# Performance work log

Hardware: AMD Instinct MI355X
Metric: run time of the kernel (lower is better)

The kernel has to match this reference:

```python
import jax, jax.numpy as jnp
import numpy as np

INF = 1.0e6  # 'infinity' for squared EDT; max real value is ~3*128^2 ~ 5e4


def edt_1d_sq(f, axis):
    """One pass of Felzenszwalb separable squared EDT along `axis`.
    d[i] = min_j f[j] + (i - j)^2  (brute-force vectorized lower envelope)."""
    f = jnp.moveaxis(f, axis, -1)
    n = f.shape[-1]
    i = jnp.arange(n, dtype=f.dtype)
    sq = (i[:, None] - i[None, :]) ** 2  # (n, n)
    d = jnp.min(f[..., None, :] + sq, axis=-1)  # (..., n)
    return jnp.moveaxis(d, -1, axis)


def compute_fg_dtm(mask):
    """Euclidean distance transform of foreground (distance to nearest background),
    matching scipy.ndimage.distance_transform_edt applied per batch element on the
    (C, X, Y, Z) mask (C==1 so the channel axis pass is the identity).
    mask: bool (B, 1, X, Y, Z) -> float32 (B, 1, X, Y, Z)."""
    def per_b(m):
        g = jnp.where(m, jnp.float32(INF), jnp.float32(0.0))
        for ax in range(m.ndim):
            g = edt_1d_sq(g, ax)
        return jnp.sqrt(g)
    return jax.lax.map(per_b, mask)


def setup_inputs() -> dict:
    key = jax.random.key(0)
    k1, k2, k3 = jax.random.split(key, 3)
    B, C, X, Y, Z = 2, 2, 128, 128, 128
    return {
        "outputs": jax.random.normal(k1, (B, C, X, Y, Z), dtype=jnp.float32),
        "outputs_dist": jax.random.normal(k2, (B, C, X, Y, Z), dtype=jnp.float32) * 10.0,
        "y": jax.random.randint(k3, (B, 1, X, Y, Z), 0, 2),
        "distance_map_weight": 1.0,
    }


def reference(outputs, outputs_dist, y, distance_map_weight):
    n_pred_ch = outputs.shape[1]
    # MONAI one_hot: (B,1,X,Y,Z) int labels -> (B,C,X,Y,Z) float
    y1h = jnp.moveaxis(jax.nn.one_hot(y[:, 0], n_pred_ch, dtype=outputs.dtype), -1, 1)
    x = outputs[:, 1:]            # foreground logits (B, 1, X, Y, Z)
    t = y1h[:, 1:]                # foreground mask
    od = outputs_dist[:, 1:]
    gt_dis = compute_fg_dtm(t > 0.5)
    # BCE with logits (mean reduction), numerically stable
    loss_ce = jnp.mean(jnp.maximum(x, 0.0) - x * t + jnp.log1p(jnp.exp(-jnp.abs(x))))
    # dice loss, flattened per batch element
    N = x.shape[0]
    smooth = jnp.float32(1.0)
    p = jax.nn.sigmoid(x).reshape(N, -1)
    tf = t.reshape(N, -1)
    dice = (2.0 * jnp.sum(p * tf, axis=1) + smooth) / (jnp.sum(p, axis=1) + jnp.sum(tf, axis=1) + smooth)
    loss_dice = 1.0 - jnp.sum(dice) / N
    # weighted L1 on the distance head, masked by the foreground mask
    msum = jnp.sum(t)
    loss_dist = jnp.where(
        msum == 0,
        jnp.float32(0.0),
        jnp.sum(jnp.abs(od - gt_dis) * t) / jnp.maximum(msum, jnp.float32(1e-12)),
    )
    return loss_ce + loss_dice + distance_map_weight * loss_dist
```

## Files before the change

### kernel.cpp

```cpp
#include <hip/hip_runtime.h>
#include <math.h>

#define M_SPATIAL 2097152

__device__ __forceinline__ float wave_redf(float v) {
#pragma unroll
  for (int o = 32; o > 0; o >>= 1) v += __shfl_down(v, o, 64);
  return v;
}
__device__ __forceinline__ double wave_redd(double v) {
#pragma unroll
  for (int o = 32; o > 0; o >>= 1) v += __shfl_down(v, o, 64);
  return v;
}
__device__ __forceinline__ float min3f(float a, float b, float c) {
  float d;
  asm("v_min3_f32 %0, %1, %2, %3" : "=v"(d) : "v"(a), "v"(b), "v"(c));
  return d;
}


__global__ __launch_bounds__(256) void kAB(const int* __restrict__ y,
                                           const float* __restrict__ outputs,
                                           float* __restrict__ g,
                                           double* __restrict__ part) {
  int blk = blockIdx.x;
  int b  = blk >> 9;
  int yy = (blk >> 2) & 127;
  int zq = blk & 3;
  int t  = threadIdx.x;
  int c  = t >> 5;
  int zl = t & 31;
  int x0 = c * 16;
  size_t sp   = (size_t)yy * 128 + (size_t)zq * 32 + zl;
  size_t base = (size_t)b * M_SPATIAL + sp;
  const float* xc = outputs + (size_t)(b * 2 + 1) * M_SPATIAL;

  int yb[16];
  float xv[16];
#pragma unroll
  for (int k = 0; k < 16; ++k) yb[k] = y[base + (size_t)(x0 + k) * 16384];
#pragma unroll
  for (int k = 0; k < 16; ++k) xv[k] = xc[sp + (size_t)(x0 + k) * 16384];

  int lastE = -200, nextE = 400;
#pragma unroll
  for (int k = 0; k < 16; ++k) lastE = (yb[k] == 1) ? lastE : (x0 + k);
#pragma unroll
  for (int k = 15; k >= 0; --k) nextE = (yb[k] == 1) ? nextE : (x0 + k);

  __shared__ int lE[8][32];
  __shared__ int nE[8][32];
  lE[c][zl] = lastE;
  nE[c][zl] = nextE;
  __syncthreads();

  int carryL = -200, carryN = 400;
#pragma unroll
  for (int q = 0; q < 7; ++q) {
    if (q < c)     carryL = max(carryL, lE[q][zl]);
    if (q + 1 > c) carryN = min(carryN, nE[q + 1][zl]);
  }

  float yy2f = (float)(yy * yy);
  float hinf = 1000000.f + yy2f;

  int df[16];
  int ll = carryL;
#pragma unroll
  for (int k = 0; k < 16; ++k) {
    ll = (yb[k] == 1) ? ll : (x0 + k);
    df[k] = min(x0 + k - ll, 200);
  }
  float ov[16];
  int nn = carryN;
#pragma unroll
  for (int k = 15; k >= 0; --k) {
    nn = (yb[k] == 1) ? nn : (x0 + k);
    int m = min(df[k], min(nn - (x0 + k), 200));
    ov[k] = (m >= 128) ? hinf : ((float)(m * m) + yy2f);
  }
#pragma unroll
  for (int k = 0; k < 16; ++k) g[base + (size_t)(x0 + k) * 16384] = ov[k];

  float ce = 0.f, ps = 0.f, pts = 0.f, tsum = 0.f;
#pragma unroll
  for (int k = 0; k < 16; ++k) {
    float tt = (yb[k] == 1) ? 1.0f : 0.0f;
    float xx = xv[k];
    ce += fmaxf(xx, 0.0f) - xx * tt + log1pf(expf(-fabsf(xx)));
    float p = 1.0f / (1.0f + expf(-xx));
    ps += p; pts += p * tt; tsum += tt;
  }
  float r0 = wave_redf(ce), r1 = wave_redf(ps), r2 = wave_redf(pts), r3 = wave_redf(tsum);
  __shared__ float sm[4][4];
  int lane = t & 63, w = t >> 6;
  if (lane == 0) { sm[w][0] = r0; sm[w][1] = r1; sm[w][2] = r2; sm[w][3] = r3; }
  __syncthreads();
  if (t == 0) {
    part[blk]        = (double)(sm[0][0] + sm[1][0] + sm[2][0] + sm[3][0]);
    part[1024 + blk] = (double)(sm[0][1] + sm[1][1] + sm[2][1] + sm[3][1]);
    part[2048 + blk] = (double)(sm[0][2] + sm[1][2] + sm[2][2] + sm[3][2]);
    part[3072 + blk] = (double)(sm[0][3] + sm[1][3] + sm[2][3] + sm[3][3]);
  }
}

__global__ __launch_bounds__(512, 1) void kCD(const float* __restrict__ g,
                                              const float* __restrict__ od,
                                              double* __restrict__ part) {
  __shared__ float hl[144 * 129];
  __shared__ float sred[8];
  int blk = blockIdx.x;
  int b = blk >> 7, xx = blk & 127;
  int t = threadIdx.x;
  size_t rb = (size_t)b * M_SPATIAL + (size_t)xx * 16384;

  for (int idx = t; idx < 8 * 129; idx += 512) {
    hl[idx] = 1.0e9f;
    hl[136 * 129 + idx] = 1.0e9f;
  }
  const float4* g4 = (const float4*)(g + rb);
#pragma unroll
  for (int r = 0; r < 8; ++r) {
    int i4 = t + r * 512;
    float4 v = g4[i4];
    int yy = i4 >> 5, z4 = (i4 & 31) * 4;
    float* p = &hl[(yy + 8) * 129 + z4];
    p[0] = v.x; p[1] = v.y; p[2] = v.z; p[3] = v.w;
  }
  __syncthreads();

  int zcol = t & 127, ig = t >> 7;
  float dvy[2][16];
#pragma unroll
  for (int cb = 0; cb < 2; ++cb) {
    int ibase = ig * 32 + cb * 16;
    float best[16], mc[16];
#pragma unroll
    for (int k = 0; k < 16; ++k) {
      best[k] = 3.0e38f;
      mc[k] = -2.0f * (float)(ibase + k);
    }
    float jb = (float)(ibase - 8);
#pragma unroll 4
    for (int p = 0; p < 16; ++p) {
      float h0 = hl[(ibase + 2 * p) * 129 + zcol];
      float h1 = hl[(ibase + 2 * p + 1) * 129 + zcol];
      float j0 = jb + (float)(2 * p), j1 = jb + (float)(2 * p + 1);
#pragma unroll
      for (int k = 0; k < 16; ++k) {
        float v0 = fmaf(mc[k], j0, h0);
        float v1 = fmaf(mc[k], j1, h1);
        best[k] = min3f(v0, v1, best[k]);
      }
    }
    int ok = 1;
#pragma unroll
    for (int k = 0; k < 16; ++k) {
      int i = ibase + k;
      dvy[cb][k] = (float)(i * i) + best[k];
      float bnd = (float)min((k + 9) * (k + 9), (24 - k) * (24 - k));
      ok &= (dvy[cb][k] <= bnd);
    }
    if (!__all(ok)) {
#pragma unroll
      for (int k = 0; k < 16; ++k) best[k] = 3.0e38f;
#pragma unroll 2
      for (int j = 0; j < 128; j += 2) {
        float h0 = hl[(j + 8) * 129 + zcol];
        float h1 = hl[(j + 9) * 129 + zcol];
        float j0 = (float)j, j1 = (float)(j + 1);
#pragma unroll
        for (int k = 0; k < 16; ++k) {
          float v0 = fmaf(mc[k], j0, h0);
          float v1 = fmaf(mc[k], j1, h1);
          best[k] = min3f(v0, v1, best[k]);
        }
      }
#pragma unroll
      for (int k = 0; k < 16; ++k) {
        int i = ibase + k;
        dvy[cb][k] = (float)(i * i) + best[k];
      }
    }
  }
  __syncthreads();
  {
    float zq = (float)(zcol * zcol);
#pragma unroll
    for (int cb = 0; cb < 2; ++cb) {
      int ibase = ig * 32 + cb * 16;
#pragma unroll
      for (int k = 0; k < 16; ++k)
        hl[(zcol + 8) * 129 + (ibase + k)] = dvy[cb][k] + zq;
    }
  }
  __syncthreads();

  int ycol = t & 127, izg = t >> 7;
  size_t odb = (size_t)(2 * b + 1) * M_SPATIAL + (size_t)xx * 16384 +
               (size_t)ycol * 128 + (size_t)izg * 32;
  const float4* o4 = (const float4*)(od + odb);
  float4 ovv[8];
#pragma unroll
  for (int r = 0; r < 8; ++r) ovv[r] = o4[r];
  const float* of = (const float*)ovv;

  float dist = 0.f;
#pragma unroll
  for (int cb = 0; cb < 2; ++cb) {
    int izb = izg * 32 + cb * 16;
    float best[16], mc[16];
#pragma unroll
    for (int k = 0; k < 16; ++k) {
      best[k] = 3.0e38f;
      mc[k] = -2.0f * (float)(izb + k);
    }
    float jb = (float)(izb - 8);
#pragma unroll 4
    for (int p = 0; p < 16; ++p) {
      float h0 = hl[(izb + 2 * p) * 129 + ycol];
      float h1 = hl[(izb + 2 * p + 1) * 129 + ycol];
      float j0 = jb + (float)(2 * p), j1 = jb + (float)(2 * p + 1);
#pragma unroll
      for (int k = 0; k < 16; ++k) {
        float v0 = fmaf(mc[k], j0, h0);
        float v1 = fmaf(mc[k], j1, h1);
        best[k] = min3f(v0, v1, best[k]);
      }
    }
    float dv[16];
    int ok = 1;
#pragma unroll
    for (int k = 0; k < 16; ++k) {
      int i = izb + k;
      dv[k] = (float)(i * i) + best[k];
      float bnd = (float)min((k + 9) * (k + 9), (24 - k) * (24 - k));
      ok &= (dv[k] <= bnd);
    }
    if (!__all(ok)) {
#pragma unroll
      for (int k = 0; k < 16; ++k) best[k] = 3.0e38f;
#pragma unroll 2
      for (int j = 0; j < 128; j += 2) {
        float h0 = hl[(j + 8) * 129 + ycol];
        float h1 = hl[(j + 9) * 129 + ycol];
        float j0 = (float)j, j1 = (float)(j + 1);
#pragma unroll
        for (int k = 0; k < 16; ++k) {
          float v0 = fmaf(mc[k], j0, h0);
          float v1 = fmaf(mc[k], j1, h1);
          best[k] = min3f(v0, v1, best[k]);
        }
      }
#pragma unroll
      for (int k = 0; k < 16; ++k) {
        int i = izb + k;
        dv[k] = (float)(i * i) + best[k];
      }
    }
#pragma unroll
    for (int k = 0; k < 16; ++k) {
      if (dv[k] > 0.f) dist += fabsf(of[cb * 16 + k] - sqrtf(dv[k]));
    }
  }
  float r = wave_redf(dist);
  int lane = t & 63, w = t >> 6;
  if (lane == 0) sred[w] = r;
  __syncthreads();
  if (t == 0) {
    float s = 0.f;
#pragma unroll
    for (int q = 0; q < 8; ++q) s += sred[q];
    part[4096 + blk] = (double)s;
  }
}

__global__ __launch_bounds__(256) void k_final(const double* __restrict__ part,
                                               const float* __restrict__ wptr,
                                               float* __restrict__ out) {
  int i = threadIdx.x;
  double ce  = part[i] + part[i + 256] + part[i + 512] + part[i + 768];
  double p0  = part[1024 + i] + part[1024 + i + 256];
  double p1  = part[1536 + i] + part[1536 + i + 256];
  double pt0 = part[2048 + i] + part[2048 + i + 256];
  double pt1 = part[2560 + i] + part[2560 + i + 256];
  double t0  = part[3072 + i] + part[3072 + i + 256];
  double t1  = part[3584 + i] + part[3584 + i + 256];
  double ds  = part[4096 + i];

  ce = wave_redd(ce); p0 = wave_redd(p0); p1 = wave_redd(p1);
  pt0 = wave_redd(pt0); pt1 = wave_redd(pt1);
  t0 = wave_redd(t0); t1 = wave_redd(t1); ds = wave_redd(ds);

  __shared__ double sm[4][8];
  int lane = threadIdx.x & 63, w = threadIdx.x >> 6;
  if (lane == 0) {
    sm[w][0] = ce; sm[w][1] = p0; sm[w][2] = p1; sm[w][3] = pt0;
    sm[w][4] = pt1; sm[w][5] = t0; sm[w][6] = t1; sm[w][7] = ds;
  }
  __syncthreads();
  if (threadIdx.x == 0) {
    double a[8];
    for (int q = 0; q < 8; ++q) a[q] = sm[0][q] + sm[1][q] + sm[2][q] + sm[3][q];
    double cem = a[0] / 4194304.0;
    double dice0 = (2.0 * a[3] + 1.0) / (a[1] + a[5] + 1.0);
    double dice1 = (2.0 * a[4] + 1.0) / (a[2] + a[6] + 1.0);
    double ldice = 1.0 - 0.5 * (dice0 + dice1);
    double msum = a[5] + a[6];
    double ldist = (msum == 0.0) ? 0.0 : a[7] / fmax(msum, 1e-12);
    out[0] = (float)(cem + ldice + (double)wptr[0] * ldist);
  }
}

extern "C" void kernel_launch(void* const* d_in, const int* in_sizes, int n_in,
                              void* d_out, int out_size, void* d_ws, size_t ws_size,
                              hipStream_t stream) {
  const float* outputs      = (const float*)d_in[0];
  const float* outputs_dist = (const float*)d_in[1];
  const int*   y            = (const int*)d_in[2];
  const float* wptr         = (const float*)d_in[3];
  float* out = (float*)d_out;

  double* part = (double*)d_ws;
  float* g = (float*)((char*)d_ws + 65536);

  kAB<<<1024, 256, 0, stream>>>(y, outputs, g, part);
  kCD<<<256, 512, 0, stream>>>(g, outputs_dist, part);
  k_final<<<1, 256, 0, stream>>>(part, wptr, out);
}
```

Measured before the change: 139.1 us.

## Stage x-pass tiles through LDS with vectorized loads and transposed intermediate layout

kAB now loads y and logits as int4/float4 contiguous along z, stages labels in shared memory, runs the x-axis scan from LDS, and writes the intermediate as float4 in a (b, y, x, z) transposed layout. kCD reads from that transposed layout. The grid is halved with each block covering 64 z columns. The goal is to replace strided scalar global accesses with coalesced vector accesses. The cost is a large shared buffer, which may reduce occupancy, plus extra barriers.

Measured after the change: 200.6 us. +44.2%, slower.

```diff
diff --git a/kernel.cpp b/kernel.cpp
--- a/kernel.cpp
+++ b/kernel.cpp
@@ -2,6 +2,7 @@
 #include <math.h>
 
 #define M_SPATIAL 2097152
+#define MV4 (M_SPATIAL / 4)
 
 __device__ __forceinline__ float wave_redf(float v) {
 #pragma unroll
@@ -20,44 +21,64 @@
 }
 
 
-__global__ __launch_bounds__(256) void kAB(const int* __restrict__ y,
-                                           const float* __restrict__ outputs,
-                                           float* __restrict__ g,
-                                           double* __restrict__ part) {
+__global__ __launch_bounds__(256, 2) void kAB(const int* __restrict__ y,
+                                              const float* __restrict__ outputs,
+                                              float* __restrict__ gT,
+                                              double* __restrict__ part) {
+  __shared__ int ysl[128 * 68];
+  __shared__ int lE[4][64];
+  __shared__ int nE[4][64];
+  __shared__ float sm[4][4];
   int blk = blockIdx.x;
-  int b  = blk >> 9;
-  int yy = (blk >> 2) & 127;
-  int zq = blk & 3;
+  int b  = blk >> 8;
+  int yy = (blk >> 1) & 127;
+  int zh = blk & 1;
   int t  = threadIdx.x;
-  int c  = t >> 5;
-  int zl = t & 31;
-  int x0 = c * 16;
-  size_t sp   = (size_t)yy * 128 + (size_t)zq * 32 + zl;
-  size_t base = (size_t)b * M_SPATIAL + sp;
-  const float* xc = outputs + (size_t)(b * 2 + 1) * M_SPATIAL;
-
-  int yb[16];
-  float xv[16];
-#pragma unroll
-  for (int k = 0; k < 16; ++k) yb[k] = y[base + (size_t)(x0 + k) * 16384];
-#pragma unroll
-  for (int k = 0; k < 16; ++k) xv[k] = xc[sp + (size_t)(x0 + k) * 16384];
+
+  const int4*   y4  = (const int4*)y;
+  const float4* xc4 = (const float4*)outputs + (size_t)(b * 2 + 1) * MV4;
+
+  float ce = 0.f, ps = 0.f, pts = 0.f, tsum = 0.f;
+#pragma unroll
+  for (int r = 0; r < 8; ++r) {
+    int i4 = t + r * 256;
+    int x  = i4 >> 4;
+    int u  = i4 & 15;
+    size_t sp4 = (size_t)x * 4096 + (size_t)yy * 32 + (size_t)zh * 16 + u;
+    int4  yv = y4[(size_t)b * MV4 + sp4];
+    float4 xv = xc4[sp4];
+#define ELEM(cc, yc)                                                        \
+    {                                                                       \
+      float tt = (yc == 1) ? 1.0f : 0.0f;                                   \
+      float xx = xv.cc;                                                     \
+      ce += fmaxf(xx, 0.0f) - xx * tt + log1pf(expf(-fabsf(xx)));           \
+      float p = 1.0f / (1.0f + expf(-xx));                                  \
+      ps += p; pts += p * tt; tsum += tt;                                   \
+    }
+    ELEM(x, yv.x) ELEM(y, yv.y) ELEM(z, yv.z) ELEM(w, yv.w)
+#undef ELEM
+    *(int4*)&ysl[x * 68 + u * 4] = yv;
+  }
+  __syncthreads();
+
+  int zl = t & 63, c = t >> 6;
+  int x0 = c * 32;
+  int yb[32];
+#pragma unroll
+  for (int k = 0; k < 32; ++k) yb[k] = ysl[(x0 + k) * 68 + zl];
 
   int lastE = -200, nextE = 400;
 #pragma unroll
-  for (int k = 0; k < 16; ++k) lastE = (yb[k] == 1) ? lastE : (x0 + k);
-#pragma unroll
-  for (int k = 15; k >= 0; --k) nextE = (yb[k] == 1) ? nextE : (x0 + k);
-
-  __shared__ int lE[8][32];
-  __shared__ int nE[8][32];
+  for (int k = 0; k < 32; ++k) lastE = (yb[k] == 1) ? lastE : (x0 + k);
+#pragma unroll
+  for (int k = 31; k >= 0; --k) nextE = (yb[k] == 1) ? nextE : (x0 + k);
   lE[c][zl] = lastE;
   nE[c][zl] = nextE;
   __syncthreads();
 
   int carryL = -200, carryN = 400;
 #pragma unroll
-  for (int q = 0; q < 7; ++q) {
+  for (int q = 0; q < 3; ++q) {
     if (q < c)     carryL = max(carryL, lE[q][zl]);
     if (q + 1 > c) carryN = min(carryN, nE[q + 1][zl]);
   }
@@ -65,47 +86,47 @@
   float yy2f = (float)(yy * yy);
   float hinf = 1000000.f + yy2f;
 
-  int df[16];
+  int df[32];
   int ll = carryL;
 #pragma unroll
-  for (int k = 0; k < 16; ++k) {
+  for (int k = 0; k < 32; ++k) {
     ll = (yb[k] == 1) ? ll : (x0 + k);
     df[k] = min(x0 + k - ll, 200);
   }
-  float ov[16];
+  float* hsl = (float*)ysl;
   int nn = carryN;
 #pragma unroll
-  for (int k = 15; k >= 0; --k) {
+  for (int k = 31; k >= 0; --k) {
     nn = (yb[k] == 1) ? nn : (x0 + k);
     int m = min(df[k], min(nn - (x0 + k), 200));
-    ov[k] = (m >= 128) ? hinf : ((float)(m * m) + yy2f);
-  }
-#pragma unroll
-  for (int k = 0; k < 16; ++k) g[base + (size_t)(x0 + k) * 16384] = ov[k];
-
-  float ce = 0.f, ps = 0.f, pts = 0.f, tsum = 0.f;
-#pragma unroll
-  for (int k = 0; k < 16; ++k) {
-    float tt = (yb[k] == 1) ? 1.0f : 0.0f;
-    float xx = xv[k];
-    ce += fmaxf(xx, 0.0f) - xx * tt + log1pf(expf(-fabsf(xx)));
-    float p = 1.0f / (1.0f + expf(-xx));
-    ps += p; pts += p * tt; tsum += tt;
-  }
+    hsl[(x0 + k) * 68 + zl] = (m >= 128) ? hinf : ((float)(m * m) + yy2f);
+  }
+  __syncthreads();
+
+  float4* gT4 = (float4*)gT;
+#pragma unroll
+  for (int r = 0; r < 8; ++r) {
+    int i4 = t + r * 256;
+    int x  = i4 >> 4;
+    int u  = i4 & 15;
+    float4 v = *(float4*)&hsl[x * 68 + u * 4];
+    gT4[(size_t)b * MV4 + (size_t)yy * 4096 + (size_t)x * 32 +
+        (size_t)zh * 16 + u] = v;
+  }
+
   float r0 = wave_redf(ce), r1 = wave_redf(ps), r2 = wave_redf(pts), r3 = wave_redf(tsum);
-  __shared__ float sm[4][4];
   int lane = t & 63, w = t >> 6;
   if (lane == 0) { sm[w][0] = r0; sm[w][1] = r1; sm[w][2] = r2; sm[w][3] = r3; }
   __syncthreads();
   if (t == 0) {
     part[blk]        = (double)(sm[0][0] + sm[1][0] + sm[2][0] + sm[3][0]);
-    part[1024 + blk] = (double)(sm[0][1] + sm[1][1] + sm[2][1] + sm[3][1]);
-    part[2048 + blk] = (double)(sm[0][2] + sm[1][2] + sm[2][2] + sm[3][2]);
-    part[3072 + blk] = (double)(sm[0][3] + sm[1][3] + sm[2][3] + sm[3][3]);
-  }
-}
-
-__global__ __launch_bounds__(512, 1) void kCD(const float* __restrict__ g,
+    part[512 + blk]  = (double)(sm[0][1] + sm[1][1] + sm[2][1] + sm[3][1]);
+    part[1024 + blk] = (double)(sm[0][2] + sm[1][2] + sm[2][2] + sm[3][2]);
+    part[1536 + blk] = (double)(sm[0][3] + sm[1][3] + sm[2][3] + sm[3][3]);
+  }
+}
+
+__global__ __launch_bounds__(512, 1) void kCD(const float* __restrict__ gT,
                                               const float* __restrict__ od,
                                               double* __restrict__ part) {
   __shared__ float hl[144 * 129];
@@ -113,19 +134,18 @@
   int blk = blockIdx.x;
   int b = blk >> 7, xx = blk & 127;
   int t = threadIdx.x;
-  size_t rb = (size_t)b * M_SPATIAL + (size_t)xx * 16384;
 
   for (int idx = t; idx < 8 * 129; idx += 512) {
     hl[idx] = 1.0e9f;
     hl[136 * 129 + idx] = 1.0e9f;
   }
-  const float4* g4 = (const float4*)(g + rb);
+  const float4* gT4 = (const float4*)gT;
 #pragma unroll
   for (int r = 0; r < 8; ++r) {
     int i4 = t + r * 512;
-    float4 v = g4[i4];
-    int yy = i4 >> 5, z4 = (i4 & 31) * 4;
-    float* p = &hl[(yy + 8) * 129 + z4];
+    int yyi = i4 >> 5, u = i4 & 31;
+    float4 v = gT4[(size_t)b * MV4 + (size_t)yyi * 4096 + (size_t)xx * 32 + u];
+    float* p = &hl[(yyi + 8) * 129 + u * 4];
     p[0] = v.x; p[1] = v.y; p[2] = v.z; p[3] = v.w;
   }
   __syncthreads();
@@ -272,7 +292,7 @@
     float s = 0.f;
 #pragma unroll
     for (int q = 0; q < 8; ++q) s += sred[q];
-    part[4096 + blk] = (double)s;
+    part[2048 + blk] = (double)s;
   }
 }
 
@@ -280,14 +300,14 @@
                                                const float* __restrict__ wptr,
                                                float* __restrict__ out) {
   int i = threadIdx.x;
-  double ce  = part[i] + part[i + 256] + part[i + 512] + part[i + 768];
-  double p0  = part[1024 + i] + part[1024 + i + 256];
-  double p1  = part[1536 + i] + part[1536 + i + 256];
-  double pt0 = part[2048 + i] + part[2048 + i + 256];
-  double pt1 = part[2560 + i] + part[2560 + i + 256];
-  double t0  = part[3072 + i] + part[3072 + i + 256];
-  double t1  = part[3584 + i] + part[3584 + i + 256];
-  double ds  = part[4096 + i];
+  double ce  = part[i] + part[i + 256];
+  double p0  = part[512 + i];
+  double p1  = part[768 + i];
+  double pt0 = part[1024 + i];
+  double pt1 = part[1280 + i];
+  double t0  = part[1536 + i];
+  double t1  = part[1792 + i];
+  double ds  = part[2048 + i];
 
   ce = wave_redd(ce); p0 = wave_redd(p0); p1 = wave_redd(p1);
   pt0 = wave_redd(pt0); pt1 = wave_redd(pt1);
@@ -323,9 +343,9 @@
   float* out = (float*)d_out;
 
   double* part = (double*)d_ws;
-  float* g = (float*)((char*)d_ws + 65536);
-
-  kAB<<<1024, 256, 0, stream>>>(y, outputs, g, part);
-  kCD<<<256, 512, 0, stream>>>(g, outputs_dist, part);
+  float* gT = (float*)((char*)d_ws + 65536);
+
+  kAB<<<512, 256, 0, stream>>>(y, outputs, gT, part);
+  kCD<<<256, 512, 0, stream>>>(gT, outputs_dist, part);
   k_final<<<1, 256, 0, stream>>>(part, wptr, out);
 }
```

## Stage kAB loads through shared memory with vectorized int4/float4 and transposed g layout

Applied to the files above, without the earlier changes.

kAB now loads y and logits as int4/float4 vectors into a shared tile, computes the BCE/dice partial sums on the vector loads, and runs the x-axis EDT from shared memory. It writes the intermediate g in a (y, x, z) transposed layout through shared memory with float4 stores, and kCD reads it with the matching indexing. The intent is to replace scalar loads and stores strided by 16384 along x with wide coalesced accesses. The cost is extra shared memory (about 18 KB per block) and an extra barrier, and kCD's reads now hit 128-byte segments strided by yy instead of contiguous rows.

Result: slower. 206.0 us (+48.1%).

```diff
diff --git a/kernel.cpp b/kernel.cpp
--- a/kernel.cpp
+++ b/kernel.cpp
@@ -2,6 +2,7 @@
 #include <math.h>
 
 #define M_SPATIAL 2097152
+#define MV4 (M_SPATIAL / 4)
 
 __device__ __forceinline__ float wave_redf(float v) {
 #pragma unroll
@@ -20,37 +21,57 @@
 }
 
 
-__global__ __launch_bounds__(256) void kAB(const int* __restrict__ y,
-                                           const float* __restrict__ outputs,
-                                           float* __restrict__ g,
-                                           double* __restrict__ part) {
+__global__ __launch_bounds__(256, 4) void kAB(const int* __restrict__ y,
+                                              const float* __restrict__ outputs,
+                                              float* __restrict__ gT,
+                                              double* __restrict__ part) {
+  __shared__ int ysl[128 * 36];
+  __shared__ int lE[8][32];
+  __shared__ int nE[8][32];
+  __shared__ float sm[4][4];
   int blk = blockIdx.x;
   int b  = blk >> 9;
   int yy = (blk >> 2) & 127;
   int zq = blk & 3;
   int t  = threadIdx.x;
-  int c  = t >> 5;
-  int zl = t & 31;
+
+  const int4*   y4  = (const int4*)y;
+  const float4* xc4 = (const float4*)outputs + (size_t)(b * 2 + 1) * MV4;
+
+  float ce = 0.f, ps = 0.f, pts = 0.f, tsum = 0.f;
+#pragma unroll
+  for (int r = 0; r < 4; ++r) {
+    int i4 = t + r * 256;
+    int x  = i4 >> 3;
+    int u  = i4 & 7;
+    size_t sp4 = (size_t)x * 4096 + (size_t)yy * 32 + (size_t)zq * 8 + u;
+    int4  yv = y4[(size_t)b * MV4 + sp4];
+    float4 xv = xc4[sp4];
+#define ELEM(cc, yc)                                                        \
+    {                                                                       \
+      float tt = (yc == 1) ? 1.0f : 0.0f;                                   \
+      float xx = xv.cc;                                                     \
+      ce += fmaxf(xx, 0.0f) - xx * tt + log1pf(expf(-fabsf(xx)));           \
+      float p = 1.0f / (1.0f + expf(-xx));                                  \
+      ps += p; pts += p * tt; tsum += tt;                                   \
+    }
+    ELEM(x, yv.x) ELEM(y, yv.y) ELEM(z, yv.z) ELEM(w, yv.w)
+#undef ELEM
+    *(int4*)&ysl[x * 36 + u * 4] = yv;
+  }
+  __syncthreads();
+
+  int zl = t & 31, c = t >> 5;
   int x0 = c * 16;
-  size_t sp   = (size_t)yy * 128 + (size_t)zq * 32 + zl;
-  size_t base = (size_t)b * M_SPATIAL + sp;
-  const float* xc = outputs + (size_t)(b * 2 + 1) * M_SPATIAL;
-
   int yb[16];
-  float xv[16];
-#pragma unroll
-  for (int k = 0; k < 16; ++k) yb[k] = y[base + (size_t)(x0 + k) * 16384];
-#pragma unroll
-  for (int k = 0; k < 16; ++k) xv[k] = xc[sp + (size_t)(x0 + k) * 16384];
+#pragma unroll
+  for (int k = 0; k < 16; ++k) yb[k] = ysl[(x0 + k) * 36 + zl];
 
   int lastE = -200, nextE = 400;
 #pragma unroll
   for (int k = 0; k < 16; ++k) lastE = (yb[k] == 1) ? lastE : (x0 + k);
 #pragma unroll
   for (int k = 15; k >= 0; --k) nextE = (yb[k] == 1) ? nextE : (x0 + k);
-
-  __shared__ int lE[8][32];
-  __shared__ int nE[8][32];
   lE[c][zl] = lastE;
   nE[c][zl] = nextE;
   __syncthreads();
@@ -72,28 +93,28 @@
     ll = (yb[k] == 1) ? ll : (x0 + k);
     df[k] = min(x0 + k - ll, 200);
   }
-  float ov[16];
+  float* hsl = (float*)ysl;
   int nn = carryN;
 #pragma unroll
   for (int k = 15; k >= 0; --k) {
     nn = (yb[k] == 1) ? nn : (x0 + k);
     int m = min(df[k], min(nn - (x0 + k), 200));
-    ov[k] = (m >= 128) ? hinf : ((float)(m * m) + yy2f);
-  }
-#pragma unroll
-  for (int k = 0; k < 16; ++k) g[base + (size_t)(x0 + k) * 16384] = ov[k];
-
-  float ce = 0.f, ps = 0.f, pts = 0.f, tsum = 0.f;
-#pragma unroll
-  for (int k = 0; k < 16; ++k) {
-    float tt = (yb[k] == 1) ? 1.0f : 0.0f;
-    float xx = xv[k];
-    ce += fmaxf(xx, 0.0f) - xx * tt + log1pf(expf(-fabsf(xx)));
-    float p = 1.0f / (1.0f + expf(-xx));
-    ps += p; pts += p * tt; tsum += tt;
-  }
+    hsl[(x0 + k) * 36 + zl] = (m >= 128) ? hinf : ((float)(m * m) + yy2f);
+  }
+  __syncthreads();
+
+  float4* gT4 = (float4*)gT;
+#pragma unroll
+  for (int r = 0; r < 4; ++r) {
+    int i4 = t + r * 256;
+    int x  = i4 >> 3;
+    int u  = i4 & 7;
+    float4 v = *(float4*)&hsl[x * 36 + u * 4];
+    gT4[(size_t)b * MV4 + (size_t)yy * 4096 + (size_t)x * 32 +
+        (size_t)zq * 8 + u] = v;
+  }
+
   float r0 = wave_redf(ce), r1 = wave_redf(ps), r2 = wave_redf(pts), r3 = wave_redf(tsum);
-  __shared__ float sm[4][4];
   int lane = t & 63, w = t >> 6;
   if (lane == 0) { sm[w][0] = r0; sm[w][1] = r1; sm[w][2] = r2; sm[w][3] = r3; }
   __syncthreads();
@@ -105,7 +126,7 @@
   }
 }
 
-__global__ __launch_bounds__(512, 1) void kCD(const float* __restrict__ g,
+__global__ __launch_bounds__(512, 1) void kCD(const float* __restrict__ gT,
                                               const float* __restrict__ od,
                                               double* __restrict__ part) {
   __shared__ float hl[144 * 129];
@@ -113,19 +134,18 @@
   int blk = blockIdx.x;
   int b = blk >> 7, xx = blk & 127;
   int t = threadIdx.x;
-  size_t rb = (size_t)b * M_SPATIAL + (size_t)xx * 16384;
 
   for (int idx = t; idx < 8 * 129; idx += 512) {
     hl[idx] = 1.0e9f;
     hl[136 * 129 + idx] = 1.0e9f;
   }
-  const float4* g4 = (const float4*)(g + rb);
+  const float4* gT4 = (const float4*)gT;
 #pragma unroll
   for (int r = 0; r < 8; ++r) {
     int i4 = t + r * 512;
-    float4 v = g4[i4];
-    int yy = i4 >> 5, z4 = (i4 & 31) * 4;
-    float* p = &hl[(yy + 8) * 129 + z4];
+    int yyi = i4 >> 5, u = i4 & 31;
+    float4 v = gT4[(size_t)b * MV4 + (size_t)yyi * 4096 + (size_t)xx * 32 + u];
+    float* p = &hl[(yyi + 8) * 129 + u * 4];
     p[0] = v.x; p[1] = v.y; p[2] = v.z; p[3] = v.w;
   }
   __syncthreads();
@@ -323,9 +343,9 @@
   float* out = (float*)d_out;
 
   double* part = (double*)d_ws;
-  float* g = (float*)((char*)d_ws + 65536);
-
-  kAB<<<1024, 256, 0, stream>>>(y, outputs, g, part);
-  kCD<<<256, 512, 0, stream>>>(g, outputs_dist, part);
+  float* gT = (float*)((char*)d_ws + 65536);
+
+  kAB<<<1024, 256, 0, stream>>>(y, outputs, gT, part);
+  kCD<<<256, 512, 0, stream>>>(gT, outputs_dist, part);
   k_final<<<1, 256, 0, stream>>>(part, wptr, out);
 }
```
